# Kernel optimization log

Measured on AMD Instinct MI355X. Metric: run time of the kernel, lower is better.

The kernel has to match this reference:

```python
import jax, jax.numpy as jnp
import numpy as np

B, S, V, E, H, C = 64, 512, 30000, 300, 256, 32


def setup_inputs() -> dict:
    key = jax.random.key(0)
    ks = jax.random.split(key, 12)
    g = 0.02
    return dict(
        tokens=jax.random.randint(ks[0], (B, S), 1, V),
        lengths=jax.random.randint(ks[1], (B,), S // 2, S + 1),
        targets=jax.random.randint(ks[2], (B, S), 0, C),
        emb=jax.random.normal(ks[3], (V, E), jnp.float32) * g,
        Wf=jax.random.normal(ks[4], (E, 4 * H), jnp.float32) * g,
        Uf=jax.random.normal(ks[5], (H, 4 * H), jnp.float32) * g,
        bf=jnp.zeros((4 * H,), jnp.float32),
        Wb=jax.random.normal(ks[6], (E, 4 * H), jnp.float32) * g,
        Ub=jax.random.normal(ks[7], (H, 4 * H), jnp.float32) * g,
        bb=jnp.zeros((4 * H,), jnp.float32),
        Wd=jax.random.normal(ks[8], (2 * H, C), jnp.float32) * g,
        bd=jnp.zeros((C,), jnp.float32),
        trans=jax.random.uniform(ks[9], (C, C), jnp.float32),
    )


def _lstm(x, W, U, b):
    # x: [B,S,E] -> hidden sequence [B,S,H]; Keras gate order i,f,g(cand),o
    xproj = jnp.einsum('bse,eh->bsh', x, W) + b  # precompute input projection

    def step(carry, xp):  # xp: [B,4H]
        h, c = carry
        z = xp + h @ U
        i, f, g, o = jnp.split(z, 4, axis=-1)
        c = jax.nn.sigmoid(f) * c + jax.nn.sigmoid(i) * jnp.tanh(g)
        h = jax.nn.sigmoid(o) * jnp.tanh(c)
        return (h, c), h

    h0 = jnp.zeros((x.shape[0], U.shape[0]), x.dtype)
    _, hs = jax.lax.scan(step, (h0, h0), jnp.swapaxes(xproj, 0, 1))
    return jnp.swapaxes(hs, 0, 1)


def _crf_log_likelihood(logits, targets, lengths, trans):
    # tfa.text.crf_log_likelihood: sequence score minus log partition (forward algorithm)
    mask = jnp.arange(S)[None, :] < lengths[:, None]  # [B,S]
    maskf = mask.astype(logits.dtype)
    unary = jnp.take_along_axis(logits, targets[..., None], axis=2)[..., 0]  # [B,S]
    unary = jnp.sum(unary * maskf, axis=1)
    binary = trans[targets[:, :-1], targets[:, 1:]] * maskf[:, 1:]  # valid where t+1 < length
    binary = jnp.sum(binary, axis=1)

    alpha0 = logits[:, 0]  # [B,C] (lengths >= 1)

    def step(alpha, inp):
        logit_t, m_t = inp  # [B,C], [B]
        new = jax.nn.logsumexp(alpha[:, :, None] + trans[None], axis=1) + logit_t
        return jnp.where(m_t[:, None], new, alpha), None

    alpha, _ = jax.lax.scan(
        step, alpha0,
        (jnp.swapaxes(logits[:, 1:], 0, 1), jnp.swapaxes(mask[:, 1:], 0, 1)))
    log_norm = jax.nn.logsumexp(alpha, axis=-1)
    return unary + binary - log_norm


def reference(tokens, lengths, targets, emb, Wf, Uf, bf, Wb, Ub, bb, Wd, bd, trans):
    x = emb[tokens]                         # [B,S,E]; dropout is identity at inference
    hf = _lstm(x, Wf, Uf, bf)               # forward direction
    hb = _lstm(x[:, ::-1], Wb, Ub, bb)[:, ::-1]  # backward direction
    h = jnp.concatenate([hf, hb], axis=-1)  # [B,S,2H]
    logits = h @ Wd + bd                    # [B,S,C]
    ll = _crf_log_likelihood(logits, targets, lengths, trans)
    return logits, ll, trans
```

## Files before the change

### kernel.cpp

```cpp
#include <hip/hip_runtime.h>

#define Bdim 64
#define Sdim 512
#define Vdim 30000
#define Edim 300
#define Hdim 256
#define Cdim 32
#define G4   1024
#define NROW 32768
#define KQ   32
#define USTAGE 9
#define RKQ    12
#define EPAIR  (Edim / 2)
#define XLSTR  152

typedef _Float16 half2v __attribute__((ext_vector_type(2)));
typedef unsigned int u32x4 __attribute__((ext_vector_type(4)));

__device__ __forceinline__ unsigned short f2h_bits(float f) {
    union { _Float16 h; unsigned short u; } v; v.h = (_Float16)f; return v.u;
}
__device__ __forceinline__ float h2f(unsigned short u) {
    union { _Float16 h; unsigned short u; } v; v.u = u; return (float)v.h;
}
__device__ __forceinline__ unsigned int pack2h(float lo, float hi) {
    return (unsigned int)f2h_bits(lo) | ((unsigned int)f2h_bits(hi) << 16);
}
__device__ __forceinline__ float sigf(float x) { return 1.0f / (1.0f + __expf(-x)); }
__device__ __forceinline__ float tanhfast(float x) { return 2.0f / (1.0f + __expf(-2.0f * x)) - 1.0f; }

__device__ __forceinline__ float dot2(unsigned int u, unsigned int h, float acc) {
#if __has_builtin(__builtin_amdgcn_fdot2)
    union { unsigned int i; half2v h; } a, b; a.i = u; b.i = h;
    return __builtin_amdgcn_fdot2(a.h, b.h, acc, false);
#else
    acc = fmaf(h2f((unsigned short)(u & 0xffffu)), h2f((unsigned short)(h & 0xffffu)), acc);
    return fmaf(h2f((unsigned short)(u >> 16)), h2f((unsigned short)(h >> 16)), acc);
#endif
}
__device__ __forceinline__ void dot8(float& a0, float& a1, u32x4 uv, u32x4 hv) {
    a0 = dot2(uv.x, hv.x, a0);
    a1 = dot2(uv.y, hv.y, a1);
    a0 = dot2(uv.z, hv.z, a0);
    a1 = dot2(uv.w, hv.w, a1);
}

__global__ __launch_bounds__(256) void k_pack_u8(
    const float* __restrict__ Uf, const float* __restrict__ Ub,
    unsigned short* __restrict__ upk8)
{
    int idx = blockIdx.x * 256 + threadIdx.x;
    if (idx >= 2 * KQ * 1024) return;
    int dir = idx >> 15;
    int rem = idx & 32767;
    int kq  = rem >> 10;
    int n   = rem & 1023;
    const float* U = dir ? Ub : Uf;
    unsigned int w[4];
    #pragma unroll
    for (int p = 0; p < 4; ++p)
        w[p] = pack2h(U[(8 * kq + 2 * p) * G4 + n], U[(8 * kq + 2 * p + 1) * G4 + n]);
    uint4 o = make_uint4(w[0], w[1], w[2], w[3]);
    *(uint4*)&upk8[(size_t)idx * 8] = o;
}

__global__ __launch_bounds__(256) void k_pack_emb(
    const float* __restrict__ emb, unsigned int* __restrict__ embp)
{
    int p = blockIdx.x * 256 + threadIdx.x;
    if (p >= Vdim * EPAIR) return;
    float2 v = *(const float2*)&emb[(size_t)2 * p];
    embp[p] = pack2h(v.x, v.y);
}

__global__ __launch_bounds__(256) void k_pack_w(
    const float* __restrict__ Wf, const float* __restrict__ Wb,
    unsigned int* __restrict__ Wp)
{
    int idx = blockIdx.x * 256 + threadIdx.x;
    if (idx >= 2 * EPAIR * 1024) return;
    int dir = idx / (EPAIR * 1024);
    int rem = idx - dir * (EPAIR * 1024);
    int kp  = rem >> 10;
    int n   = rem & 1023;
    const float* W = dir ? Wb : Wf;
    Wp[idx] = pack2h(W[(2 * kp) * G4 + n], W[(2 * kp + 1) * G4 + n]);
}

__global__ __launch_bounds__(256) void k_pack_wd(
    const float* __restrict__ Wd, unsigned int* __restrict__ WdP)
{
    int i = blockIdx.x * 256 + threadIdx.x;
    if (i >= 256 * 32) return;
    int kp = i >> 5, c = i & 31;
    WdP[i] = pack2h(Wd[(2 * kp) * 32 + c], Wd[(2 * kp + 1) * 32 + c]);
}

__global__ __launch_bounds__(256) void k_xproj(
    const int* __restrict__ tokens, const unsigned int* __restrict__ embp,
    const unsigned int* __restrict__ Wp,
    const float* __restrict__ bf_, const float* __restrict__ bb_,
    unsigned short* __restrict__ xp)
{
    __shared__ unsigned int xl[32 * XLSTR];
    const int m0  = blockIdx.x * 32;
    const int tid = threadIdx.x;

    for (int i = tid; i < 32 * EPAIR; i += 256) {
        int r = i / EPAIR, kp = i - r * EPAIR;
        int tok = tokens[m0 + r];
        xl[r * XLSTR + kp] = embp[(size_t)tok * EPAIR + kp];
    }
    __syncthreads();

    const int tx = tid & 31, ty = tid >> 5;
    const int c0 = blockIdx.y * 128 + tx * 4;
    float bj[2][4];
    #pragma unroll
    for (int j = 0; j < 4; ++j) {
        bj[0][j] = bf_[c0 + j];
        bj[1][j] = bb_[c0 + j];
    }
    float acc[2][4][4] = {};

    for (int kp = 0; kp < EPAIR; kp += 2) {
        uint2 xv[4];
        #pragma unroll
        for (int i = 0; i < 4; ++i)
            xv[i] = *(const uint2*)&xl[(ty * 4 + i) * XLSTR + kp];
        #pragma unroll
        for (int kk = 0; kk < 2; ++kk) {
            #pragma unroll
            for (int d = 0; d < 2; ++d) {
                uint4 wv = *(const uint4*)(Wp + (size_t)d * EPAIR * 1024
                                              + (size_t)(kp + kk) * 1024 + c0);
                #pragma unroll
                for (int i = 0; i < 4; ++i) {
                    unsigned int xpair = kk ? xv[i].y : xv[i].x;
                    acc[d][i][0] = dot2(wv.x, xpair, acc[d][i][0]);
                    acc[d][i][1] = dot2(wv.y, xpair, acc[d][i][1]);
                    acc[d][i][2] = dot2(wv.z, xpair, acc[d][i][2]);
                    acc[d][i][3] = dot2(wv.w, xpair, acc[d][i][3]);
                }
            }
        }
    }
    #pragma unroll
    for (int d = 0; d < 2; ++d) {
        size_t base = (size_t)d * NROW * G4;
        #pragma unroll
        for (int i = 0; i < 4; ++i) {
            size_t row = (size_t)(m0 + ty * 4 + i) * G4;
            ushort4 o;
            o.x = f2h_bits(acc[d][i][0] + bj[d][0]);
            o.y = f2h_bits(acc[d][i][1] + bj[d][1]);
            o.z = f2h_bits(acc[d][i][2] + bj[d][2]);
            o.w = f2h_bits(acc[d][i][3] + bj[d][3]);
            *(ushort4*)&xp[base + row + c0] = o;
        }
    }
}

__global__ __launch_bounds__(1024) void k_lstm(
    const unsigned short* __restrict__ upk8,
    const unsigned short* __restrict__ xp,
    unsigned short* __restrict__ hout)
{
    const int bx  = blockIdx.x;
    const int dir = bx >> 6;
    const int b   = bx & 63;
    const int n   = threadIdx.x;
    const int gi  = n >> 8;
    const unsigned short* __restrict__ Uq = upk8 + (size_t)dir * (KQ * 1024 * 8);
    const unsigned short* __restrict__ xpd =
        xp + (size_t)dir * NROW * G4 + (size_t)b * Sdim * G4;

    __shared__ float          abuf[1024];
    __shared__ __align__(16) unsigned short hl[256];
    extern __shared__ __align__(16) unsigned short ust[];

    {
        const u32x4* src = (const u32x4*)Uq;
        u32x4*       dst = (u32x4*)ust;
        for (int i = n; i < USTAGE * 1024; i += 1024) dst[i] = src[i];
    }
    u32x4 ur[RKQ];
    #pragma unroll
    for (int r = 0; r < RKQ; ++r)
        ur[r] = *(const u32x4*)&Uq[((size_t)(USTAGE + r) * 1024 + n) * 8];

    if (n < 256) hl[n] = 0;
    float c = 0.0f;
    __syncthreads();

    for (int step = 0; step < Sdim; ++step) {
        const int t = dir ? (Sdim - 1 - step) : step;
        float zx = h2f(xpd[(size_t)t * G4 + n]);
        float a0 = 0.0f, a1 = 0.0f;
        #pragma unroll
        for (int kq = USTAGE + RKQ; kq < KQ; ++kq) {
            u32x4 uv = *(const u32x4*)&Uq[((size_t)kq * 1024 + n) * 8];
            u32x4 hv = *(const u32x4*)&hl[kq * 8];
            dot8(a0, a1, uv, hv);
        }
        #pragma unroll
        for (int r = 0; r < RKQ; ++r) {
            u32x4 hv = *(const u32x4*)&hl[(USTAGE + r) * 8];
            dot8(a0, a1, ur[r], hv);
        }
        #pragma unroll
        for (int kq = 0; kq < USTAGE; ++kq) {
            u32x4 uv = *(const u32x4*)&ust[(kq * 1024 + n) * 8];
            u32x4 hv = *(const u32x4*)&hl[kq * 8];
            dot8(a0, a1, uv, hv);
        }
        float z = zx + a0 + a1;
        float a = (gi == 2) ? tanhfast(z) : sigf(z);
        abuf[n] = a;
        __syncthreads();
        if (n < 256) {
            float iv = abuf[n];
            float fv = abuf[n + 256];
            float gv = abuf[n + 512];
            float ov = abuf[n + 768];
            c = fv * c + iv * gv;
            float hn = ov * tanhfast(c);
            unsigned short hb = f2h_bits(hn);
            hl[n] = hb;
            hout[((size_t)(b * Sdim + t)) * 512 + dir * 256 + n] = hb;
        }
        __syncthreads();
    }
}

__global__ __launch_bounds__(256) void k_dense(
    const unsigned short* __restrict__ hall, const unsigned int* __restrict__ WdP,
    const float* __restrict__ bd, float* __restrict__ outL)
{
    __shared__ unsigned int wlT[32 * 260];
    __shared__ unsigned int hu[8 * 256];
    const int r0  = blockIdx.x * 8;
    const int tid = threadIdx.x;

    for (int i = tid; i < 256 * 32; i += 256) {
        int kp = i >> 5, c = i & 31;
        wlT[c * 260 + kp] = WdP[i];
    }
    const unsigned int* hsrc = (const unsigned int*)(hall + (size_t)r0 * 512);
    for (int i = tid; i < 8 * 256; i += 256) hu[i] = hsrc[i];
    __syncthreads();

    const int tx = tid & 31, ty = tid >> 5;
    float a0 = 0.0f, a1 = 0.0f;
    #pragma unroll 8
    for (int kp = 0; kp < 256; kp += 4) {
        u32x4 hv = *(const u32x4*)&hu[ty * 256 + kp];
        u32x4 wv = *(const u32x4*)&wlT[tx * 260 + kp];
        a0 = dot2(wv.x, hv.x, a0);
        a1 = dot2(wv.y, hv.y, a1);
        a0 = dot2(wv.z, hv.z, a0);
        a1 = dot2(wv.w, hv.w, a1);
    }
    outL[(size_t)(r0 + ty) * 32 + tx] = a0 + a1 + bd[tx];
}

__global__ __launch_bounds__(64) void k_crf(
    const float* __restrict__ logits, const int* __restrict__ targets,
    const int* __restrict__ lengths, const float* __restrict__ trans,
    float* __restrict__ out_ll, float* __restrict__ out_trans)
{
    const int b    = blockIdx.x;
    const int lane = threadIdx.x;
    __shared__ __align__(16) float alpha[32];

    if (b == 0)
        for (int i = lane; i < 1024; i += 64) out_trans[i] = trans[i];

    const int len = lengths[b];
    const float* lg = logits + (size_t)b * Sdim * Cdim;
    const int*   tg = targets + b * Sdim;

    float ub = 0.0f;
    for (int t = lane; t < Sdim; t += 64) {
        if (t < len) {
            ub += lg[t * 32 + tg[t]];
            if (t >= 1) ub += trans[tg[t - 1] * 32 + tg[t]];
        }
    }
    #pragma unroll
    for (int m = 32; m >= 1; m >>= 1) ub += __shfl_xor(ub, m);

    const int j = lane & 31, half = lane >> 5;
    float trow16[16];
    #pragma unroll
    for (int q = 0; q < 16; ++q) trow16[q] = trans[(half * 16 + q) * 32 + j];

    if (lane < 32) alpha[lane] = lg[lane];
    __syncthreads();

    float lcur = (len > 1) ? lg[32 + j] : 0.0f;
    for (int t = 1; t < len; ++t) {
        float lnxt = (t + 1 < len) ? lg[(t + 1) * 32 + j] : 0.0f;
        float v[16];
        #pragma unroll
        for (int q = 0; q < 16; ++q) v[q] = alpha[half * 16 + q] + trow16[q];
        float m0 = v[0], m1 = v[1], m2 = v[2], m3 = v[3];
        #pragma unroll
        for (int q = 4; q < 16; q += 4) {
            m0 = fmaxf(m0, v[q]);
            m1 = fmaxf(m1, v[q + 1]);
            m2 = fmaxf(m2, v[q + 2]);
            m3 = fmaxf(m3, v[q + 3]);
        }
        float ml = fmaxf(fmaxf(m0, m1), fmaxf(m2, m3));
        float m  = fmaxf(ml, __shfl_xor(ml, 32));
        float s0 = 0.0f, s1 = 0.0f, s2 = 0.0f, s3 = 0.0f;
        #pragma unroll
        for (int q = 0; q < 16; q += 4) {
            s0 += __expf(v[q] - m);
            s1 += __expf(v[q + 1] - m);
            s2 += __expf(v[q + 2] - m);
            s3 += __expf(v[q + 3] - m);
        }
        float sl = (s0 + s1) + (s2 + s3);
        float s  = sl + __shfl_xor(sl, 32);
        float nv = m + __logf(s) + lcur;
        __syncthreads();
        if (lane < 32) alpha[lane] = nv;
        __syncthreads();
        lcur = lnxt;
    }
    if (lane == 0) {
        float m = -3.0e38f;
        for (int q = 0; q < 32; ++q) m = fmaxf(m, alpha[q]);
        float s = 0.0f;
        for (int q = 0; q < 32; ++q) s += __expf(alpha[q] - m);
        out_ll[b] = ub - (m + __logf(s));
    }
}

extern "C" void kernel_launch(void* const* d_in, const int* in_sizes, int n_in,
                              void* d_out, int out_size, void* d_ws, size_t ws_size,
                              hipStream_t stream) {
    (void)in_sizes; (void)n_in; (void)out_size; (void)ws_size;
    const int*   tokens  = (const int*)d_in[0];
    const int*   lengths = (const int*)d_in[1];
    const int*   targets = (const int*)d_in[2];
    const float* emb     = (const float*)d_in[3];
    const float* Wf      = (const float*)d_in[4];
    const float* Uf      = (const float*)d_in[5];
    const float* bf_     = (const float*)d_in[6];
    const float* Wb      = (const float*)d_in[7];
    const float* Ub      = (const float*)d_in[8];
    const float* bb_     = (const float*)d_in[9];
    const float* Wd      = (const float*)d_in[10];
    const float* bd      = (const float*)d_in[11];
    const float* trans   = (const float*)d_in[12];

    float* out_logits = (float*)d_out;
    float* out_ll     = out_logits + 1048576;
    float* out_trans  = out_ll + 64;

    char* ws = (char*)d_ws;
    unsigned short* upk8 = (unsigned short*)ws;
    unsigned short* xp   = (unsigned short*)(ws + (1u << 20));
    char*           hreg = ws + (1u << 20) + (size_t)2 * NROW * G4 * 2;
    unsigned short* hall = (unsigned short*)hreg;
    unsigned int*   embp = (unsigned int*)hreg;
    unsigned int*   Wp   = (unsigned int*)(hreg + (size_t)Vdim * EPAIR * 4);
    unsigned int*   WdP  = (unsigned int*)ws;

    const size_t lstm_dyn_lds = (size_t)USTAGE * 1024 * 8 * 2;

    k_pack_u8 <<<dim3(256), dim3(256), 0, stream>>>(Uf, Ub, upk8);
    k_pack_emb<<<dim3((Vdim * EPAIR + 255) / 256), dim3(256), 0, stream>>>(emb, embp);
    k_pack_w  <<<dim3((2 * EPAIR * 1024 + 255) / 256), dim3(256), 0, stream>>>(Wf, Wb, Wp);
    k_xproj   <<<dim3(NROW / 32, 8), dim3(256), 0, stream>>>(tokens, embp, Wp, bf_, bb_, xp);
    k_lstm    <<<dim3(128), dim3(1024), lstm_dyn_lds, stream>>>(upk8, xp, hall);
    k_pack_wd <<<dim3(32), dim3(256), 0, stream>>>(Wd, WdP);
    k_dense   <<<dim3(NROW / 8), dim3(256), 0, stream>>>(hall, WdP, bd, out_logits);
    k_crf     <<<dim3(64), dim3(64), 0, stream>>>(out_logits, targets, lengths, trans, out_ll, out_trans);
}
```

Baseline: 1.431 ms.

## Rewrite input projection GEMM with MFMA f16 tiles and per-direction grid

Replaces the packed-dot2 scalar GEMM in the input projection kernel with an LDS-tiled MFMA 16x16x32 f16 matrix multiply over 64x128 tiles, splitting the two directions across a z grid dimension. The embedding gather now loads in K chunks into shared memory, with zero padding past the 150 pairs. The aim is to move the large token-by-4H projection onto matrix cores instead of vector ALUs. In exchange it adds K padding waste, unvectorized strided output stores of single halves, and a barrier-synchronized load/compute loop with no double buffering.

```diff
diff --git a/kernel.cpp b/kernel.cpp
--- a/kernel.cpp
+++ b/kernel.cpp
@@ -12,9 +12,11 @@
 #define USTAGE 9
 #define RKQ    12
 #define EPAIR  (Edim / 2)
-#define XLSTR  152
+#define KCH    5
 
 typedef _Float16 half2v __attribute__((ext_vector_type(2)));
+typedef _Float16 f16x8  __attribute__((ext_vector_type(8)));
+typedef float    f32x4  __attribute__((ext_vector_type(4)));
 typedef unsigned int u32x4 __attribute__((ext_vector_type(4)));
 
 __device__ __forceinline__ unsigned short f2h_bits(float f) {
@@ -96,67 +98,97 @@
     WdP[i] = pack2h(Wd[(2 * kp) * 32 + c], Wd[(2 * kp + 1) * 32 + c]);
 }
 
-__global__ __launch_bounds__(256) void k_xproj(
+__global__ __launch_bounds__(256, 4) void k_xproj(
     const int* __restrict__ tokens, const unsigned int* __restrict__ embp,
     const unsigned int* __restrict__ Wp,
     const float* __restrict__ bf_, const float* __restrict__ bb_,
     unsigned short* __restrict__ xp)
 {
-    __shared__ unsigned int xl[32 * XLSTR];
-    const int m0  = blockIdx.x * 32;
+    __shared__ unsigned short As[64][72];
+    __shared__ unsigned short Bs[128][72];
+    __shared__ int tokL[64];
+
+    const int m0  = blockIdx.x * 64;
+    const int n0  = blockIdx.y * 128;
+    const int dir = blockIdx.z;
+    const unsigned int* W = Wp + (size_t)dir * EPAIR * 1024;
+    const float* bias = dir ? bb_ : bf_;
     const int tid = threadIdx.x;
 
-    for (int i = tid; i < 32 * EPAIR; i += 256) {
-        int r = i / EPAIR, kp = i - r * EPAIR;
-        int tok = tokens[m0 + r];
-        xl[r * XLSTR + kp] = embp[(size_t)tok * EPAIR + kp];
-    }
+    if (tid < 64) tokL[tid] = tokens[m0 + tid];
     __syncthreads();
 
-    const int tx = tid & 31, ty = tid >> 5;
-    const int c0 = blockIdx.y * 128 + tx * 4;
-    float bj[2][4];
-    #pragma unroll
-    for (int j = 0; j < 4; ++j) {
-        bj[0][j] = bf_[c0 + j];
-        bj[1][j] = bb_[c0 + j];
-    }
-    float acc[2][4][4] = {};
-
-    for (int kp = 0; kp < EPAIR; kp += 2) {
-        uint2 xv[4];
-        #pragma unroll
-        for (int i = 0; i < 4; ++i)
-            xv[i] = *(const uint2*)&xl[(ty * 4 + i) * XLSTR + kp];
-        #pragma unroll
-        for (int kk = 0; kk < 2; ++kk) {
+    const int w    = tid >> 6;
+    const int wm   = w >> 1;
+    const int wn   = w & 1;
+    const int lane = tid & 63;
+    const int lr   = lane & 15;
+    const int lh   = lane >> 4;
+
+    f32x4 acc[2][4] = {};
+
+    float bv[4];
+    #pragma unroll
+    for (int nt = 0; nt < 4; ++nt)
+        bv[nt] = bias[n0 + wn * 64 + nt * 16 + lr];
+
+    for (int kc = 0; kc < KCH; ++kc) {
+        const int k0p = kc * 32;
+        if (kc) __syncthreads();
+
+        {
+            const int r  = tid >> 2;
+            const int jb = (tid & 3) * 8;
+            const int tok = tokL[r];
+            unsigned int* dst = (unsigned int*)&As[r][0];
             #pragma unroll
-            for (int d = 0; d < 2; ++d) {
-                uint4 wv = *(const uint4*)(Wp + (size_t)d * EPAIR * 1024
-                                              + (size_t)(kp + kk) * 1024 + c0);
-                #pragma unroll
-                for (int i = 0; i < 4; ++i) {
-                    unsigned int xpair = kk ? xv[i].y : xv[i].x;
-                    acc[d][i][0] = dot2(wv.x, xpair, acc[d][i][0]);
-                    acc[d][i][1] = dot2(wv.y, xpair, acc[d][i][1]);
-                    acc[d][i][2] = dot2(wv.z, xpair, acc[d][i][2]);
-                    acc[d][i][3] = dot2(wv.w, xpair, acc[d][i][3]);
-                }
+            for (int q = 0; q < 8; ++q) {
+                int gp = k0p + jb + q;
+                dst[jb + q] = (gp < EPAIR) ? embp[(size_t)tok * EPAIR + gp] : 0u;
             }
         }
-    }
-    #pragma unroll
-    for (int d = 0; d < 2; ++d) {
-        size_t base = (size_t)d * NROW * G4;
-        #pragma unroll
-        for (int i = 0; i < 4; ++i) {
-            size_t row = (size_t)(m0 + ty * 4 + i) * G4;
-            ushort4 o;
-            o.x = f2h_bits(acc[d][i][0] + bj[d][0]);
-            o.y = f2h_bits(acc[d][i][1] + bj[d][1]);
-            o.z = f2h_bits(acc[d][i][2] + bj[d][2]);
-            o.w = f2h_bits(acc[d][i][3] + bj[d][3]);
-            *(ushort4*)&xp[base + row + c0] = o;
+        {
+            #pragma unroll
+            for (int q = 0; q < 16; ++q) {
+                int ii = q * 256 + tid;
+                int jp = ii >> 7;
+                int c  = ii & 127;
+                int gp = k0p + jp;
+                unsigned int v = (gp < EPAIR) ? W[(size_t)gp * 1024 + n0 + c] : 0u;
+                ((unsigned int*)&Bs[c][0])[jp] = v;
+            }
+        }
+        __syncthreads();
+
+        f16x8 a[2][2];
+        #pragma unroll
+        for (int mt = 0; mt < 2; ++mt)
+            #pragma unroll
+            for (int ks = 0; ks < 2; ++ks)
+                a[mt][ks] = *(const f16x8*)&As[wm * 32 + mt * 16 + lr][ks * 32 + lh * 8];
+        #pragma unroll
+        for (int nt = 0; nt < 4; ++nt) {
+            f16x8 b0 = *(const f16x8*)&Bs[wn * 64 + nt * 16 + lr][lh * 8];
+            f16x8 b1 = *(const f16x8*)&Bs[wn * 64 + nt * 16 + lr][32 + lh * 8];
+            #pragma unroll
+            for (int mt = 0; mt < 2; ++mt) {
+                acc[mt][nt] = __builtin_amdgcn_mfma_f32_16x16x32_f16(a[mt][0], b0, acc[mt][nt], 0, 0, 0);
+                acc[mt][nt] = __builtin_amdgcn_mfma_f32_16x16x32_f16(a[mt][1], b1, acc[mt][nt], 0, 0, 0);
+            }
+        }
+    }
+
+    size_t base = (size_t)dir * NROW * G4;
+    #pragma unroll
+    for (int mt = 0; mt < 2; ++mt) {
+        #pragma unroll
+        for (int nt = 0; nt < 4; ++nt) {
+            int col = n0 + wn * 64 + nt * 16 + lr;
+            #pragma unroll
+            for (int rr = 0; rr < 4; ++rr) {
+                int row = m0 + wm * 32 + mt * 16 + lh * 4 + rr;
+                xp[base + (size_t)row * G4 + col] = f2h_bits(acc[mt][nt][rr] + bv[nt]);
+            }
         }
     }
 }
@@ -375,7 +407,7 @@
     k_pack_u8 <<<dim3(256), dim3(256), 0, stream>>>(Uf, Ub, upk8);
     k_pack_emb<<<dim3((Vdim * EPAIR + 255) / 256), dim3(256), 0, stream>>>(emb, embp);
     k_pack_w  <<<dim3((2 * EPAIR * 1024 + 255) / 256), dim3(256), 0, stream>>>(Wf, Wb, Wp);
-    k_xproj   <<<dim3(NROW / 32, 8), dim3(256), 0, stream>>>(tokens, embp, Wp, bf_, bb_, xp);
+    k_xproj   <<<dim3(NROW / 64, 8, 2), dim3(256), 0, stream>>>(tokens, embp, Wp, bf_, bb_, xp);
     k_lstm    <<<dim3(128), dim3(1024), lstm_dyn_lds, stream>>>(upk8, xp, hall);
     k_pack_wd <<<dim3(32), dim3(256), 0, stream>>>(Wd, WdP);
     k_dense   <<<dim3(NROW / 8), dim3(256), 0, stream>>>(hall, WdP, bd, out_logits);
```

Result: faster. 1.179 ms (-17.6%).
